# Kernel tuning notes

Hardware: AMD Instinct MI355X
Metric: run time of the kernel (lower is better)

Reference implementation:

```python
import jax, jax.numpy as jnp
import numpy as np

N_NODES = 100000
N_EDGES = 1600000
IN_DIM = 64
OUT_DIM = 64
K_HEADS = 4
HEAD_DIM = OUT_DIM // K_HEADS


def setup_inputs() -> dict:
    key = jax.random.key(0)
    ks = jax.random.split(key, 12)
    x = jax.random.normal(ks[0], (N_NODES, IN_DIM), dtype=jnp.float32)
    edge_index = jax.random.randint(ks[1], (2, N_EDGES), 0, N_NODES, dtype=jnp.int64)
    edge_sign = jax.random.randint(ks[2], (N_EDGES,), 0, 2, dtype=jnp.int64)
    s = 1.0 / np.sqrt(IN_DIM)
    Wl_w = jax.random.uniform(ks[3], (OUT_DIM, IN_DIM), minval=-s, maxval=s, dtype=jnp.float32)
    Wl_b = jax.random.uniform(ks[4], (OUT_DIM,), minval=-s, maxval=s, dtype=jnp.float32)
    sign_tab = jax.random.normal(ks[5], (2, HEAD_DIM), dtype=jnp.float32)
    so = 1.0 / np.sqrt(OUT_DIM)
    Wh_w = jax.random.uniform(ks[6], (OUT_DIM, OUT_DIM), minval=-so, maxval=so, dtype=jnp.float32)
    Wh_b = jax.random.uniform(ks[7], (OUT_DIM,), minval=-so, maxval=so, dtype=jnp.float32)
    mlp_w1 = jax.random.uniform(ks[8], (OUT_DIM, OUT_DIM), minval=-so, maxval=so, dtype=jnp.float32)
    mlp_b1 = jax.random.uniform(ks[9], (OUT_DIM,), minval=-so, maxval=so, dtype=jnp.float32)
    mlp_w2 = jax.random.uniform(ks[10], (OUT_DIM, OUT_DIM), minval=-so, maxval=so, dtype=jnp.float32)
    mlp_b2 = jax.random.uniform(ks[11], (OUT_DIM,), minval=-so, maxval=so, dtype=jnp.float32)
    eps = jnp.zeros((1,), dtype=jnp.float32)
    return {"x": x, "edge_index": edge_index, "edge_sign": edge_sign,
            "Wl_w": Wl_w, "Wl_b": Wl_b, "sign_tab": sign_tab,
            "Wh_w": Wh_w, "Wh_b": Wh_b, "mlp_w1": mlp_w1, "mlp_b1": mlp_b1,
            "mlp_w2": mlp_w2, "mlp_b2": mlp_b2, "eps": eps}


def reference(x, edge_index, edge_sign, Wl_w, Wl_b, sign_tab, Wh_w, Wh_b,
              mlp_w1, mlp_b1, mlp_w2, mlp_b2, eps):
    N = x.shape[0]
    row, col = edge_index[0], edge_index[1]
    h = x @ Wl_w.T + Wl_b                              # [N, out_dim]
    hr = h.reshape(N, K_HEADS, HEAD_DIM)               # [N, K, hd]
    h_i = hr[row]                                      # [E, K, hd]
    h_j = hr[col]                                      # [E, K, hd]
    s_emb = sign_tab[edge_sign][:, None, :]            # [E, 1, hd]
    score = jnp.sum(h_i * h_j * s_emb, axis=-1)        # [E, K]
    # segment softmax over edges grouped by target node (row)
    mx = jax.ops.segment_max(score, row, num_segments=N)
    mx = jnp.where(jnp.isfinite(mx), mx, 0.0)          # empty segments -> 0
    ex = jnp.exp(score - mx[row])                      # [E, K]
    den = jax.ops.segment_sum(ex, row, num_segments=N)
    alpha = ex / (den[row] + 1e-16)                    # [E, K]
    # scatter-add weighted messages per head (vectorized over heads)
    msg = h_j * alpha[:, :, None]                      # [E, K, hd]
    aggr = jax.ops.segment_sum(msg, row, num_segments=N)  # [N, K, hd]
    m_l = aggr.reshape(N, OUT_DIM) @ Wh_w.T + Wh_b
    z = (1.0 + eps) * h + m_l
    hid = jax.nn.relu(z @ mlp_w1.T + mlp_b1)
    return hid @ mlp_w2.T + mlp_b2
```

## Files before the change

### kernel.cpp

```cpp
#include <hip/hip_runtime.h>

#define DIM 64
#define NBUCK 256
#define BSHIFT 9
#define BCAP 12288
#define CHUNK 4096

typedef __attribute__((ext_vector_type(4))) float f32x4;
typedef __attribute__((ext_vector_type(2))) float f32x2v;
typedef __attribute__((ext_vector_type(8))) short short8;

#define MFMA16(a, b, c) __builtin_amdgcn_mfma_f32_16x16x32_bf16(a, b, c, 0, 0, 0)

template <int CTRL>
__device__ __forceinline__ float qperm(float v) {
    return __int_as_float(__builtin_amdgcn_update_dpp(
        0, __float_as_int(v), CTRL, 0xF, 0xF, true));
}

__device__ __forceinline__ void cvt8(const float* f, short8& hi, short8& lo) {
#pragma unroll
    for (int e = 0; e < 8; ++e) {
        const unsigned u = __float_as_uint(f[e]);
        hi[e] = (short)(u >> 16);
        const float hf = __uint_as_float(u & 0xFFFF0000u);
        lo[e] = (short)(__float_as_uint(f[e] - hf) >> 16);
    }
}

__device__ __forceinline__ unsigned short bf16rne(float f) {
    const unsigned u = __float_as_uint(f);
    return (unsigned short)((u + 0x7FFFu + ((u >> 16) & 1u)) >> 16);
}

__global__ __launch_bounds__(256) void prep_kernel(
    const float* __restrict__ Wl, const float* __restrict__ Wh,
    const float* __restrict__ W1, const float* __restrict__ W2,
    short8* __restrict__ wf, int* __restrict__ bcursor,
    int* __restrict__ edata, int* __restrict__ offsets, int N, int E)
{
    const int tid = threadIdx.x;
    bcursor[tid] = 0;
    edata[E + tid] = 0;
    edata[E + 256 + tid] = 0;
    if (tid == 0) offsets[N] = E;
    const int m = tid >> 6, l = tid & 63;
    const float* W = (m == 0) ? Wl : (m == 1) ? Wh : (m == 2) ? W1 : W2;
    const int o = l & 15;
    const int kg = (l >> 4) * 8;
#pragma unroll
    for (int t = 0; t < 4; ++t)
#pragma unroll
        for (int s = 0; s < 2; ++s) {
            float f[8];
#pragma unroll
            for (int e = 0; e < 8; ++e)
                f[e] = W[(o + 16 * t) * DIM + 32 * s + kg + e];
            short8 hi, lo;
            cvt8(f, hi, lo);
            const int base = (((m * 4 + t) * 2 + s) * 2);
            wf[(base + 0) * 64 + l] = hi;
            wf[(base + 1) * 64 + l] = lo;
        }
}

__global__ __launch_bounds__(256, 3) void gemmbin_kernel(
    const float* __restrict__ x, const short8* __restrict__ wf,
    const float* __restrict__ bias, float* __restrict__ h,
    unsigned short* __restrict__ hb, int N,
    const int* __restrict__ ei, const int* __restrict__ sgn,
    int* __restrict__ bcursor, int* __restrict__ records, int E, int NB)
{
    if (blockIdx.x & 1) {
        const int l = threadIdx.x & 63;
        const int gw = (blockIdx.x >> 1) * 4 + (threadIdx.x >> 6);
        const int nw = NB * 4;
        const int nstrips = (N + 15) >> 4;
        const int lr = l & 15, lk = (l >> 4) * 8, lrow4 = (l >> 4) * 4;

        short8 wh_[4][2], wl_[4][2];
#pragma unroll
        for (int t = 0; t < 4; ++t)
#pragma unroll
            for (int s = 0; s < 2; ++s) {
                wh_[t][s] = wf[(((0 * 4 + t) * 2 + s) * 2 + 0) * 64 + l];
                wl_[t][s] = wf[(((0 * 4 + t) * 2 + s) * 2 + 1) * 64 + l];
            }
        float b4[4];
#pragma unroll
        for (int t = 0; t < 4; ++t) b4[t] = bias[lr + 16 * t];

        for (int strip = gw; strip < nstrips; strip += nw) {
            const int rbase = strip * 16;
            const int arow = min(rbase + lr, N - 1);
            short8 ah[2], al[2];
#pragma unroll
            for (int s = 0; s < 2; ++s) {
                const float4 p0 = *reinterpret_cast<const float4*>(x + (size_t)arow * DIM + 32 * s + lk);
                const float4 p1 = *reinterpret_cast<const float4*>(x + (size_t)arow * DIM + 32 * s + lk + 4);
                float f[8] = {p0.x, p0.y, p0.z, p0.w, p1.x, p1.y, p1.z, p1.w};
                cvt8(f, ah[s], al[s]);
            }
            f32x4 acc[4];
#pragma unroll
            for (int t = 0; t < 4; ++t) acc[t] = (f32x4){b4[t], b4[t], b4[t], b4[t]};
#pragma unroll
            for (int s = 0; s < 2; ++s) {
#pragma unroll
                for (int t = 0; t < 4; ++t) acc[t] = MFMA16(ah[s], wh_[t][s], acc[t]);
#pragma unroll
                for (int t = 0; t < 4; ++t) acc[t] = MFMA16(ah[s], wl_[t][s], acc[t]);
#pragma unroll
                for (int t = 0; t < 4; ++t) acc[t] = MFMA16(al[s], wh_[t][s], acc[t]);
            }
#pragma unroll
            for (int t = 0; t < 4; ++t)
#pragma unroll
                for (int rg = 0; rg < 4; ++rg) {
                    const int row = rbase + lrow4 + rg;
                    if (row < N) {
                        h[(size_t)row * DIM + lr + 16 * t] = acc[t][rg];
                        hb[(size_t)row * DIM + lr + 16 * t] = bf16rne(acc[t][rg]);
                    }
                }
        }
    } else {
        const int tid = threadIdx.x;
        const int base = (blockIdx.x >> 1) * CHUNK;
        __shared__ int lcnt[NBUCK];
        __shared__ int lbase[NBUCK];
        lcnt[tid] = 0;
        __syncthreads();
        const int lim = min(CHUNK, E - base);
        if (lim == CHUNK && (E & 3) == 0) {
            int r[16];
#pragma unroll
            for (int j = 0; j < 4; ++j) {
                const int4 a = *(reinterpret_cast<const int4*>(ei + base) + tid * 4 + j);
                r[4*j+0]=a.x; r[4*j+1]=a.y; r[4*j+2]=a.z; r[4*j+3]=a.w;
            }
#pragma unroll
            for (int i = 0; i < 16; ++i) atomicAdd(&lcnt[r[i] >> BSHIFT], 1);
            __syncthreads();
            const int c = lcnt[tid];
            lbase[tid] = c ? atomicAdd(&bcursor[tid], c) : 0;
            lcnt[tid] = 0;
            __syncthreads();
            int cc[16], ss[16];
#pragma unroll
            for (int j = 0; j < 4; ++j) {
                const int4 a = *(reinterpret_cast<const int4*>(ei + E + base) + tid * 4 + j);
                cc[4*j+0]=a.x; cc[4*j+1]=a.y; cc[4*j+2]=a.z; cc[4*j+3]=a.w;
                const int4 s2 = *(reinterpret_cast<const int4*>(sgn + base) + tid * 4 + j);
                ss[4*j+0]=s2.x; ss[4*j+1]=s2.y; ss[4*j+2]=s2.z; ss[4*j+3]=s2.w;
            }
#pragma unroll
            for (int half = 0; half < 2; ++half) {
                int idx[8];
#pragma unroll
                for (int i = 0; i < 8; ++i) {
                    const int e8 = half * 8 + i;
                    const int bkt = r[e8] >> BSHIFT;
                    idx[i] = lbase[bkt] + atomicAdd(&lcnt[bkt], 1);
                }
#pragma unroll
                for (int i = 0; i < 8; ++i) {
                    const int e8 = half * 8 + i;
                    const int bkt = r[e8] >> BSHIFT;
                    records[bkt * BCAP + min(idx[i], BCAP - 1)] =
                        cc[e8] | (ss[e8] << 17) | ((r[e8] & 511) << 18);
                }
            }
        } else {
            for (int k = tid; k < lim; k += 256)
                atomicAdd(&lcnt[ei[base + k] >> BSHIFT], 1);
            __syncthreads();
            const int c = lcnt[tid];
            lbase[tid] = c ? atomicAdd(&bcursor[tid], c) : 0;
            lcnt[tid] = 0;
            __syncthreads();
            for (int k = tid; k < lim; k += 256) {
                const int e = base + k;
                const int rr = ei[e];
                const int cc2 = ei[E + e];
                const int s = sgn[e];
                const int b = rr >> BSHIFT;
                const int idx = min(lbase[b] + atomicAdd(&lcnt[b], 1), BCAP - 1);
                records[b * BCAP + idx] = cc2 | (s << 17) | ((rr & 511) << 18);
            }
        }
    }
}

__device__ __forceinline__ int wave_incl_scan(int v, int lane) {
#pragma unroll
    for (int off = 1; off < 64; off <<= 1) {
        int t = __shfl_up(v, (unsigned)off, 64);
        if (lane >= off) v += t;
    }
    return v;
}

__global__ __launch_bounds__(256) void build_kernel(
    const int* __restrict__ records, const int* __restrict__ bcursor,
    int* __restrict__ offsets, int* __restrict__ edata, int N)
{
    const int b = blockIdx.x;
    const int tid = threadIdx.x, lane = tid & 63, w = tid >> 6;
    const int nbase = b << BSHIFT;
    const int nn = min(512, N - nbase);
    if (nn <= 0) return;

    __shared__ int ncnt[512];
    __shared__ int wtot[8];
    __shared__ int csrb_l[NBUCK];
    __shared__ int stag[BCAP];

    {
        const int bv = min(bcursor[tid], BCAP);
        const int inc = wave_incl_scan(bv, lane);
        if (lane == 63) wtot[w] = inc;
        __syncthreads();
        int add = 0;
#pragma unroll
        for (int i = 0; i < 4; ++i)
            if (i < w) add += wtot[i];
        csrb_l[tid] = add + inc - bv;
        __syncthreads();
    }
    const int base_csr = csrb_l[b];
    const int cnt = min(bcursor[b], BCAP);
    const int* rec = records + b * BCAP;

    ncnt[tid] = 0; ncnt[256 + tid] = 0;
    __syncthreads();
    for (int i = tid; i < cnt; i += 256)
        atomicAdd(&ncnt[rec[i] >> 18], 1);
    __syncthreads();
    const int v0 = ncnt[tid], v1 = ncnt[256 + tid];
    const int i0 = wave_incl_scan(v0, lane);
    if (lane == 63) wtot[w] = i0;
    const int i1 = wave_incl_scan(v1, lane);
    if (lane == 63) wtot[4 + w] = i1;
    __syncthreads();
    int a0 = 0, a1 = 0;
#pragma unroll
    for (int i = 0; i < 4; ++i) {
        if (i < w) { a0 += wtot[i]; a1 += wtot[4 + i]; }
    }
    const int half = wtot[0] + wtot[1] + wtot[2] + wtot[3];
    const int e0 = a0 + i0 - v0;
    const int e1 = half + a1 + i1 - v1;
    if (tid < nn)       offsets[nbase + tid]       = base_csr + e0;
    if (256 + tid < nn) offsets[nbase + 256 + tid] = base_csr + e1;
    __syncthreads();
    ncnt[tid] = e0; ncnt[256 + tid] = e1;
    __syncthreads();
    for (int i = tid; i < cnt; i += 256) {
        const int rcd = rec[i];
        const int p = atomicAdd(&ncnt[rcd >> 18], 1);
        stag[p] = (rcd & 0x1FFFF) | (((rcd >> 17) & 1) << 20);
    }
    __syncthreads();
    for (int i = tid; i < cnt; i += 256)
        edata[base_csr + i] = stag[i];
}

__global__ __launch_bounds__(256) void attn_kernel(
    const float* __restrict__ h, const unsigned short* __restrict__ hb,
    const int* __restrict__ offsets, const int* __restrict__ edata,
    const float* __restrict__ sign_tab, float* __restrict__ aggr, int n)
{
    const int lane = threadIdx.x & 63;
    const int gl   = lane & 15;
    const int node = blockIdx.x * 16 + ((threadIdx.x >> 6) << 2) + (lane >> 4);
    const bool alive = node < n;
    const int nidx = alive ? node : 0;

    const int beg = offsets[nidx];
    const int deg = offsets[nidx + 1] - beg;

    const float4 hi = *reinterpret_cast<const float4*>(h + ((unsigned)nidx << 6) + (gl << 2));
    const float4 s0 = *reinterpret_cast<const float4*>(sign_tab + ((gl & 3) << 2));
    const float4 s1 = *reinterpret_cast<const float4*>(sign_tab + 16 + ((gl & 3) << 2));
    const f32x2v hs0a = {hi.x * s0.x, hi.y * s0.y};
    const f32x2v hs0b = {hi.z * s0.z, hi.w * s0.w};
    const f32x2v hs1a = {hi.x * s1.x, hi.y * s1.y};
    const f32x2v hs1b = {hi.z * s1.z, hi.w * s1.w};

    int maxdeg = max(deg, __shfl_xor(deg, 16, 64));
    maxdeg = max(maxdeg, __shfl_xor(maxdeg, 32, 64));

    float den = 0.f;
    f32x2v ma = {0.f, 0.f}, mb = {0.f, 0.f};
    const unsigned glb = (unsigned)(gl << 3);

    for (int e = 0; e < maxdeg; e += 8) {
        int pk[8];
#pragma unroll
        for (int u = 0; u < 8; ++u)
            pk[u] = edata[(unsigned)(beg + e + u)];
        uint2 v[8];
#pragma unroll
        for (int u = 0; u < 8; ++u) {
            unsigned off = (((unsigned)pk[u] & 0x1FFFFu) << 7) + glb;
            off = (e + u < deg) ? off : glb;
            v[u] = *reinterpret_cast<const uint2*>(
                reinterpret_cast<const char*>(hb) + off);
        }
#pragma unroll
        for (int u = 0; u < 8; ++u) {
            const f32x2v ha = {__uint_as_float(v[u].x << 16),
                               __uint_as_float(v[u].x & 0xFFFF0000u)};
            const f32x2v hc = {__uint_as_float(v[u].y << 16),
                               __uint_as_float(v[u].y & 0xFFFF0000u)};
            const bool sg = (pk[u] >> 20) & 1;
            const f32x2v wa = sg ? hs1a : hs0a;
            const f32x2v wb = sg ? hs1b : hs0b;
            const f32x2v p = wa * ha + wb * hc;
            float sc = p.x + p.y;
            sc += qperm<0xB1>(sc);
            sc += qperm<0x4E>(sc);
            const float ex = (e + u < deg) ? __expf(sc) : 0.f;
            den += ex;
            ma += ex * ha;
            mb += ex * hc;
        }
    }

    if (alive) {
        const float inv = 1.0f / (den + 1e-16f);
        float4 o = make_float4(ma.x * inv, ma.y * inv, mb.x * inv, mb.y * inv);
        *reinterpret_cast<float4*>(aggr + ((unsigned)node << 6) + (gl << 2)) = o;
    }
}

__global__ __launch_bounds__(256, 2) void tail_kernel(
    const float* __restrict__ aggr, const float* __restrict__ hres,
    const short8* __restrict__ wf,
    const float* __restrict__ bh, const float* __restrict__ b1,
    const float* __restrict__ b2, const float* __restrict__ eps,
    float* __restrict__ out, int N)
{
    __shared__ float zb[4][16 * 68];
    const int l = threadIdx.x & 63;
    const int w = threadIdx.x >> 6;
    const int gw = blockIdx.x * 4 + w;
    const int nw = gridDim.x * 4;
    const int nstrips = (N + 15) >> 4;
    const int lr = l & 15, lk = (l >> 4) * 8, lrow4 = (l >> 4) * 4;
    float* zw = zb[w];

    short8 whh[4][2], w1h[4][2], w2h[4][2];
#pragma unroll
    for (int t = 0; t < 4; ++t)
#pragma unroll
        for (int s = 0; s < 2; ++s) {
            whh[t][s] = wf[(((1 * 4 + t) * 2 + s) * 2 + 0) * 64 + l];
            w1h[t][s] = wf[(((2 * 4 + t) * 2 + s) * 2 + 0) * 64 + l];
            w2h[t][s] = wf[(((3 * 4 + t) * 2 + s) * 2 + 0) * 64 + l];
        }
    float bh4[4], b14[4], b24[4];
#pragma unroll
    for (int t = 0; t < 4; ++t) {
        bh4[t] = bh[lr + 16 * t];
        b14[t] = b1[lr + 16 * t];
        b24[t] = b2[lr + 16 * t];
    }
    const float escale = 1.0f + eps[0];

    for (int strip = gw; strip < nstrips; strip += nw) {
        const int rbase = strip * 16;

        float vh[4][4];
#pragma unroll
        for (int t = 0; t < 4; ++t)
#pragma unroll
            for (int rg = 0; rg < 4; ++rg)
                vh[t][rg] = hres[(size_t)min(rbase + lrow4 + rg, N - 1) * DIM + lr + 16 * t];

        const int arow = min(rbase + lr, N - 1);
        short8 ah[2], al[2];
#pragma unroll
        for (int s = 0; s < 2; ++s) {
            const float4 p0 = *reinterpret_cast<const float4*>(aggr + (size_t)arow * DIM + 32 * s + lk);
            const float4 p1 = *reinterpret_cast<const float4*>(aggr + (size_t)arow * DIM + 32 * s + lk + 4);
            float f[8] = {p0.x, p0.y, p0.z, p0.w, p1.x, p1.y, p1.z, p1.w};
            cvt8(f, ah[s], al[s]);
        }
        short8 lo_[4][2];
#pragma unroll
        for (int t = 0; t < 4; ++t)
#pragma unroll
            for (int s = 0; s < 2; ++s)
                lo_[t][s] = wf[(((1 * 4 + t) * 2 + s) * 2 + 1) * 64 + l];
        f32x4 acc[4];
#pragma unroll
        for (int t = 0; t < 4; ++t) acc[t] = (f32x4){bh4[t], bh4[t], bh4[t], bh4[t]};
#pragma unroll
        for (int s = 0; s < 2; ++s) {
#pragma unroll
            for (int t = 0; t < 4; ++t) acc[t] = MFMA16(ah[s], whh[t][s], acc[t]);
#pragma unroll
            for (int t = 0; t < 4; ++t) acc[t] = MFMA16(ah[s], lo_[t][s], acc[t]);
#pragma unroll
            for (int t = 0; t < 4; ++t) acc[t] = MFMA16(al[s], whh[t][s], acc[t]);
        }
#pragma unroll
        for (int t = 0; t < 4; ++t)
#pragma unroll
            for (int rg = 0; rg < 4; ++rg)
                zw[(lrow4 + rg) * 68 + lr + 16 * t] = fmaf(escale, vh[t][rg], acc[t][rg]);
        asm volatile("s_waitcnt lgkmcnt(0)" ::: "memory");

        short8 zh[2], zl[2];
#pragma unroll
        for (int s = 0; s < 2; ++s) {
            const float4 q0 = *reinterpret_cast<const float4*>(zw + lr * 68 + 32 * s + lk);
            const float4 q1 = *reinterpret_cast<const float4*>(zw + lr * 68 + 32 * s + lk + 4);
            float f[8] = {q0.x, q0.y, q0.z, q0.w, q1.x, q1.y, q1.z, q1.w};
            cvt8(f, zh[s], zl[s]);
        }
#pragma unroll
        for (int t = 0; t < 4; ++t)
#pragma unroll
            for (int s = 0; s < 2; ++s)
                lo_[t][s] = wf[(((2 * 4 + t) * 2 + s) * 2 + 1) * 64 + l];
#pragma unroll
        for (int t = 0; t < 4; ++t) acc[t] = (f32x4){b14[t], b14[t], b14[t], b14[t]};
#pragma unroll
        for (int s = 0; s < 2; ++s) {
#pragma unroll
            for (int t = 0; t < 4; ++t) acc[t] = MFMA16(zh[s], w1h[t][s], acc[t]);
#pragma unroll
            for (int t = 0; t < 4; ++t) acc[t] = MFMA16(zh[s], lo_[t][s], acc[t]);
#pragma unroll
            for (int t = 0; t < 4; ++t) acc[t] = MFMA16(zl[s], w1h[t][s], acc[t]);
        }
#pragma unroll
        for (int t = 0; t < 4; ++t)
#pragma unroll
            for (int rg = 0; rg < 4; ++rg)
                zw[(lrow4 + rg) * 68 + lr + 16 * t] = fmaxf(acc[t][rg], 0.f);
        asm volatile("s_waitcnt lgkmcnt(0)" ::: "memory");

        short8 hh[2], hl[2];
#pragma unroll
        for (int s = 0; s < 2; ++s) {
            const float4 q0 = *reinterpret_cast<const float4*>(zw + lr * 68 + 32 * s + lk);
            const float4 q1 = *reinterpret_cast<const float4*>(zw + lr * 68 + 32 * s + lk + 4);
            float f[8] = {q0.x, q0.y, q0.z, q0.w, q1.x, q1.y, q1.z, q1.w};
            cvt8(f, hh[s], hl[s]);
        }
#pragma unroll
        for (int t = 0; t < 4; ++t)
#pragma unroll
            for (int s = 0; s < 2; ++s)
                lo_[t][s] = wf[(((3 * 4 + t) * 2 + s) * 2 + 1) * 64 + l];
#pragma unroll
        for (int t = 0; t < 4; ++t) acc[t] = (f32x4){b24[t], b24[t], b24[t], b24[t]};
#pragma unroll
        for (int s = 0; s < 2; ++s) {
#pragma unroll
            for (int t = 0; t < 4; ++t) acc[t] = MFMA16(hh[s], w2h[t][s], acc[t]);
#pragma unroll
            for (int t = 0; t < 4; ++t) acc[t] = MFMA16(hh[s], lo_[t][s], acc[t]);
#pragma unroll
            for (int t = 0; t < 4; ++t) acc[t] = MFMA16(hl[s], w2h[t][s], acc[t]);
        }
#pragma unroll
        for (int t = 0; t < 4; ++t)
#pragma unroll
            for (int rg = 0; rg < 4; ++rg) {
                const int row = rbase + lrow4 + rg;
                if (row < N) out[(size_t)row * DIM + lr + 16 * t] = acc[t][rg];
            }
    }
}

extern "C" void kernel_launch(void* const* d_in, const int* in_sizes, int n_in,
                              void* d_out, int out_size, void* d_ws, size_t ws_size,
                              hipStream_t stream) {
    const float* x        = (const float*)d_in[0];
    const int*   ei       = (const int*)d_in[1];
    const int*   esign    = (const int*)d_in[2];
    const float* Wl_w     = (const float*)d_in[3];
    const float* Wl_b     = (const float*)d_in[4];
    const float* sign_tab = (const float*)d_in[5];
    const float* Wh_w     = (const float*)d_in[6];
    const float* Wh_b     = (const float*)d_in[7];
    const float* w1       = (const float*)d_in[8];
    const float* b1       = (const float*)d_in[9];
    const float* w2       = (const float*)d_in[10];
    const float* b2       = (const float*)d_in[11];
    const float* eps      = (const float*)d_in[12];
    float* out = (float*)d_out;

    const int N = in_sizes[0] / DIM;
    const int E = in_sizes[2];

    float* h       = (float*)d_ws;
    float* aggr    = h + (size_t)N * DIM;
    int*   records = (int*)aggr;
    int*   edata   = (int*)(aggr + (size_t)N * DIM);
    int*   bcursor = edata + (E + 520);
    int*   offsets = bcursor + NBUCK;
    short8* wf     = (short8*)(offsets + ((N + 1 + 3) & ~3));
    unsigned short* hb = (unsigned short*)d_out;

    const int NB = (E + CHUNK - 1) / CHUNK;

    prep_kernel<<<1, 256, 0, stream>>>(Wl_w, Wh_w, w1, w2, wf, bcursor,
                                       edata, offsets, N, E);

    gemmbin_kernel<<<2 * NB, 256, 0, stream>>>(x, wf, Wl_b, h, hb, N,
                                               ei, esign, bcursor, records, E, NB);

    build_kernel<<<NBUCK, 256, 0, stream>>>(records, bcursor, offsets, edata, N);

    attn_kernel<<<(N + 15) / 16, 256, 0, stream>>>(h, hb, offsets, edata, sign_tab, aggr, N);

    tail_kernel<<<512, 256, 0, stream>>>(aggr, h, wf, Wh_b, b1, b2, eps, out, N);
}
```

Baseline: 122.2 us.

## Fuse attention aggregation and MLP tail into one kernel via LDS staging

Merges the attention kernel and the tail GEMM kernel so each 16-node block keeps its aggregated rows in shared memory and runs the three 64x64 split-bf16 MFMA layers in place, with each wave owning one 16-column output tile. This removes the global write and re-read of the aggr buffer and one kernel launch. The bf16 copy of h moves from the output buffer into workspace to avoid aliasing with the fused output writes. In exchange, every block reloads weight fragments and uses extra block-wide barriers, and the tail work is no longer spread over a persistent grid.

Result: faster. 110.5 us (-9.6%).

```diff
diff --git a/kernel.cpp b/kernel.cpp
--- a/kernel.cpp
+++ b/kernel.cpp
@@ -266,15 +266,24 @@
         edata[base_csr + i] = stag[i];
 }
 
-__global__ __launch_bounds__(256) void attn_kernel(
+__global__ __launch_bounds__(256) void attntail_kernel(
     const float* __restrict__ h, const unsigned short* __restrict__ hb,
     const int* __restrict__ offsets, const int* __restrict__ edata,
-    const float* __restrict__ sign_tab, float* __restrict__ aggr, int n)
+    const float* __restrict__ sign_tab, const short8* __restrict__ wf,
+    const float* __restrict__ bh, const float* __restrict__ b1,
+    const float* __restrict__ b2, const float* __restrict__ eps,
+    float* __restrict__ out, int N)
 {
+    __shared__ float bufA[16 * 68];
+    __shared__ float bufB[16 * 68];
+
     const int lane = threadIdx.x & 63;
+    const int w    = threadIdx.x >> 6;
     const int gl   = lane & 15;
-    const int node = blockIdx.x * 16 + ((threadIdx.x >> 6) << 2) + (lane >> 4);
-    const bool alive = node < n;
+    const int g    = lane >> 4;
+    const int rbase = blockIdx.x * 16;
+    const int node  = rbase + (w << 2) + g;
+    const bool alive = node < N;
     const int nidx = alive ? node : 0;
 
     const int beg = offsets[nidx];
@@ -327,154 +336,92 @@
             mb += ex * hc;
         }
     }
-
-    if (alive) {
+    {
         const float inv = 1.0f / (den + 1e-16f);
-        float4 o = make_float4(ma.x * inv, ma.y * inv, mb.x * inv, mb.y * inv);
-        *reinterpret_cast<float4*>(aggr + ((unsigned)node << 6) + (gl << 2)) = o;
-    }
-}
-
-__global__ __launch_bounds__(256, 2) void tail_kernel(
-    const float* __restrict__ aggr, const float* __restrict__ hres,
-    const short8* __restrict__ wf,
-    const float* __restrict__ bh, const float* __restrict__ b1,
-    const float* __restrict__ b2, const float* __restrict__ eps,
-    float* __restrict__ out, int N)
-{
-    __shared__ float zb[4][16 * 68];
-    const int l = threadIdx.x & 63;
-    const int w = threadIdx.x >> 6;
-    const int gw = blockIdx.x * 4 + w;
-    const int nw = gridDim.x * 4;
-    const int nstrips = (N + 15) >> 4;
-    const int lr = l & 15, lk = (l >> 4) * 8, lrow4 = (l >> 4) * 4;
-    float* zw = zb[w];
-
-    short8 whh[4][2], w1h[4][2], w2h[4][2];
-#pragma unroll
-    for (int t = 0; t < 4; ++t)
-#pragma unroll
-        for (int s = 0; s < 2; ++s) {
-            whh[t][s] = wf[(((1 * 4 + t) * 2 + s) * 2 + 0) * 64 + l];
-            w1h[t][s] = wf[(((2 * 4 + t) * 2 + s) * 2 + 0) * 64 + l];
-            w2h[t][s] = wf[(((3 * 4 + t) * 2 + s) * 2 + 0) * 64 + l];
-        }
-    float bh4[4], b14[4], b24[4];
-#pragma unroll
-    for (int t = 0; t < 4; ++t) {
-        bh4[t] = bh[lr + 16 * t];
-        b14[t] = b1[lr + 16 * t];
-        b24[t] = b2[lr + 16 * t];
-    }
+        float* rowp = bufA + ((w << 2) + g) * 68 + (gl << 2);
+        rowp[0] = ma.x * inv; rowp[1] = ma.y * inv;
+        rowp[2] = mb.x * inv; rowp[3] = mb.y * inv;
+    }
+    __syncthreads();
+
+    const int lr = lane & 15, lk = (lane >> 4) * 8, lrow4 = (lane >> 4) * 4;
+    short8 f1h[2], f1l[2], f2h[2], f2l[2], f3h[2], f3l[2];
+#pragma unroll
+    for (int s = 0; s < 2; ++s) {
+        f1h[s] = wf[(((1 * 4 + w) * 2 + s) * 2 + 0) * 64 + lane];
+        f1l[s] = wf[(((1 * 4 + w) * 2 + s) * 2 + 1) * 64 + lane];
+        f2h[s] = wf[(((2 * 4 + w) * 2 + s) * 2 + 0) * 64 + lane];
+        f2l[s] = wf[(((2 * 4 + w) * 2 + s) * 2 + 1) * 64 + lane];
+        f3h[s] = wf[(((3 * 4 + w) * 2 + s) * 2 + 0) * 64 + lane];
+        f3l[s] = wf[(((3 * 4 + w) * 2 + s) * 2 + 1) * 64 + lane];
+    }
+    const float bhv = bh[lr + 16 * w];
+    const float b1v = b1[lr + 16 * w];
+    const float b2v = b2[lr + 16 * w];
     const float escale = 1.0f + eps[0];
 
-    for (int strip = gw; strip < nstrips; strip += nw) {
-        const int rbase = strip * 16;
-
-        float vh[4][4];
-#pragma unroll
-        for (int t = 0; t < 4; ++t)
-#pragma unroll
-            for (int rg = 0; rg < 4; ++rg)
-                vh[t][rg] = hres[(size_t)min(rbase + lrow4 + rg, N - 1) * DIM + lr + 16 * t];
-
-        const int arow = min(rbase + lr, N - 1);
-        short8 ah[2], al[2];
-#pragma unroll
-        for (int s = 0; s < 2; ++s) {
-            const float4 p0 = *reinterpret_cast<const float4*>(aggr + (size_t)arow * DIM + 32 * s + lk);
-            const float4 p1 = *reinterpret_cast<const float4*>(aggr + (size_t)arow * DIM + 32 * s + lk + 4);
-            float f[8] = {p0.x, p0.y, p0.z, p0.w, p1.x, p1.y, p1.z, p1.w};
-            cvt8(f, ah[s], al[s]);
-        }
-        short8 lo_[4][2];
-#pragma unroll
-        for (int t = 0; t < 4; ++t)
-#pragma unroll
-            for (int s = 0; s < 2; ++s)
-                lo_[t][s] = wf[(((1 * 4 + t) * 2 + s) * 2 + 1) * 64 + l];
-        f32x4 acc[4];
-#pragma unroll
-        for (int t = 0; t < 4; ++t) acc[t] = (f32x4){bh4[t], bh4[t], bh4[t], bh4[t]};
-#pragma unroll
-        for (int s = 0; s < 2; ++s) {
-#pragma unroll
-            for (int t = 0; t < 4; ++t) acc[t] = MFMA16(ah[s], whh[t][s], acc[t]);
-#pragma unroll
-            for (int t = 0; t < 4; ++t) acc[t] = MFMA16(ah[s], lo_[t][s], acc[t]);
-#pragma unroll
-            for (int t = 0; t < 4; ++t) acc[t] = MFMA16(al[s], whh[t][s], acc[t]);
-        }
-#pragma unroll
-        for (int t = 0; t < 4; ++t)
-#pragma unroll
-            for (int rg = 0; rg < 4; ++rg)
-                zw[(lrow4 + rg) * 68 + lr + 16 * t] = fmaf(escale, vh[t][rg], acc[t][rg]);
-        asm volatile("s_waitcnt lgkmcnt(0)" ::: "memory");
-
-        short8 zh[2], zl[2];
-#pragma unroll
-        for (int s = 0; s < 2; ++s) {
-            const float4 q0 = *reinterpret_cast<const float4*>(zw + lr * 68 + 32 * s + lk);
-            const float4 q1 = *reinterpret_cast<const float4*>(zw + lr * 68 + 32 * s + lk + 4);
-            float f[8] = {q0.x, q0.y, q0.z, q0.w, q1.x, q1.y, q1.z, q1.w};
-            cvt8(f, zh[s], zl[s]);
-        }
-#pragma unroll
-        for (int t = 0; t < 4; ++t)
-#pragma unroll
-            for (int s = 0; s < 2; ++s)
-                lo_[t][s] = wf[(((2 * 4 + t) * 2 + s) * 2 + 1) * 64 + l];
-#pragma unroll
-        for (int t = 0; t < 4; ++t) acc[t] = (f32x4){b14[t], b14[t], b14[t], b14[t]};
-#pragma unroll
-        for (int s = 0; s < 2; ++s) {
-#pragma unroll
-            for (int t = 0; t < 4; ++t) acc[t] = MFMA16(zh[s], w1h[t][s], acc[t]);
-#pragma unroll
-            for (int t = 0; t < 4; ++t) acc[t] = MFMA16(zh[s], lo_[t][s], acc[t]);
-#pragma unroll
-            for (int t = 0; t < 4; ++t) acc[t] = MFMA16(zl[s], w1h[t][s], acc[t]);
-        }
-#pragma unroll
-        for (int t = 0; t < 4; ++t)
-#pragma unroll
-            for (int rg = 0; rg < 4; ++rg)
-                zw[(lrow4 + rg) * 68 + lr + 16 * t] = fmaxf(acc[t][rg], 0.f);
-        asm volatile("s_waitcnt lgkmcnt(0)" ::: "memory");
-
-        short8 hh[2], hl[2];
-#pragma unroll
-        for (int s = 0; s < 2; ++s) {
-            const float4 q0 = *reinterpret_cast<const float4*>(zw + lr * 68 + 32 * s + lk);
-            const float4 q1 = *reinterpret_cast<const float4*>(zw + lr * 68 + 32 * s + lk + 4);
-            float f[8] = {q0.x, q0.y, q0.z, q0.w, q1.x, q1.y, q1.z, q1.w};
-            cvt8(f, hh[s], hl[s]);
-        }
-#pragma unroll
-        for (int t = 0; t < 4; ++t)
-#pragma unroll
-            for (int s = 0; s < 2; ++s)
-                lo_[t][s] = wf[(((3 * 4 + t) * 2 + s) * 2 + 1) * 64 + l];
-#pragma unroll
-        for (int t = 0; t < 4; ++t) acc[t] = (f32x4){b24[t], b24[t], b24[t], b24[t]};
-#pragma unroll
-        for (int s = 0; s < 2; ++s) {
-#pragma unroll
-            for (int t = 0; t < 4; ++t) acc[t] = MFMA16(hh[s], w2h[t][s], acc[t]);
-#pragma unroll
-            for (int t = 0; t < 4; ++t) acc[t] = MFMA16(hh[s], lo_[t][s], acc[t]);
-#pragma unroll
-            for (int t = 0; t < 4; ++t) acc[t] = MFMA16(hl[s], w2h[t][s], acc[t]);
-        }
-#pragma unroll
-        for (int t = 0; t < 4; ++t)
-#pragma unroll
-            for (int rg = 0; rg < 4; ++rg) {
-                const int row = rbase + lrow4 + rg;
-                if (row < N) out[(size_t)row * DIM + lr + 16 * t] = acc[t][rg];
-            }
+    float vh[4];
+#pragma unroll
+    for (int rg = 0; rg < 4; ++rg)
+        vh[rg] = h[(size_t)min(rbase + lrow4 + rg, N - 1) * DIM + lr + 16 * w];
+
+    short8 ah[2], al[2];
+#pragma unroll
+    for (int s = 0; s < 2; ++s) {
+        float f[8];
+#pragma unroll
+        for (int e = 0; e < 8; ++e) f[e] = bufA[lr * 68 + 32 * s + lk + e];
+        cvt8(f, ah[s], al[s]);
+    }
+    f32x4 acc = (f32x4){bhv, bhv, bhv, bhv};
+#pragma unroll
+    for (int s = 0; s < 2; ++s) {
+        acc = MFMA16(ah[s], f1h[s], acc);
+        acc = MFMA16(ah[s], f1l[s], acc);
+        acc = MFMA16(al[s], f1h[s], acc);
+    }
+#pragma unroll
+    for (int rg = 0; rg < 4; ++rg)
+        bufB[(lrow4 + rg) * 68 + lr + 16 * w] = fmaf(escale, vh[rg], acc[rg]);
+    __syncthreads();
+
+#pragma unroll
+    for (int s = 0; s < 2; ++s) {
+        float f[8];
+#pragma unroll
+        for (int e = 0; e < 8; ++e) f[e] = bufB[lr * 68 + 32 * s + lk + e];
+        cvt8(f, ah[s], al[s]);
+    }
+    acc = (f32x4){b1v, b1v, b1v, b1v};
+#pragma unroll
+    for (int s = 0; s < 2; ++s) {
+        acc = MFMA16(ah[s], f2h[s], acc);
+        acc = MFMA16(ah[s], f2l[s], acc);
+        acc = MFMA16(al[s], f2h[s], acc);
+    }
+#pragma unroll
+    for (int rg = 0; rg < 4; ++rg)
+        bufA[(lrow4 + rg) * 68 + lr + 16 * w] = fmaxf(acc[rg], 0.f);
+    __syncthreads();
+
+#pragma unroll
+    for (int s = 0; s < 2; ++s) {
+        float f[8];
+#pragma unroll
+        for (int e = 0; e < 8; ++e) f[e] = bufA[lr * 68 + 32 * s + lk + e];
+        cvt8(f, ah[s], al[s]);
+    }
+    acc = (f32x4){b2v, b2v, b2v, b2v};
+#pragma unroll
+    for (int s = 0; s < 2; ++s) {
+        acc = MFMA16(ah[s], f3h[s], acc);
+        acc = MFMA16(ah[s], f3l[s], acc);
+        acc = MFMA16(al[s], f3h[s], acc);
+    }
+#pragma unroll
+    for (int rg = 0; rg < 4; ++rg) {
+        const int row = rbase + lrow4 + rg;
+        if (row < N) out[(size_t)row * DIM + lr + 16 * w] = acc[rg];
     }
 }
 
@@ -498,17 +445,15 @@
 
     const int N = in_sizes[0] / DIM;
     const int E = in_sizes[2];
-
-    float* h       = (float*)d_ws;
-    float* aggr    = h + (size_t)N * DIM;
-    int*   records = (int*)aggr;
-    int*   edata   = (int*)(aggr + (size_t)N * DIM);
-    int*   bcursor = edata + (E + 520);
-    int*   offsets = bcursor + NBUCK;
-    short8* wf     = (short8*)(offsets + ((N + 1 + 3) & ~3));
-    unsigned short* hb = (unsigned short*)d_out;
-
     const int NB = (E + CHUNK - 1) / CHUNK;
+
+    float* h            = (float*)d_ws;
+    unsigned short* hb  = (unsigned short*)(h + (size_t)N * DIM);
+    int*   records      = (int*)(hb + (size_t)N * DIM);
+    int*   edata        = records + NBUCK * BCAP;
+    int*   bcursor      = edata + (E + 520);
+    int*   offsets      = bcursor + NBUCK;
+    short8* wf          = (short8*)(offsets + ((N + 1 + 3) & ~3));
 
     prep_kernel<<<1, 256, 0, stream>>>(Wl_w, Wh_w, w1, w2, wf, bcursor,
                                        edata, offsets, N, E);
@@ -518,7 +463,6 @@
 
     build_kernel<<<NBUCK, 256, 0, stream>>>(records, bcursor, offsets, edata, N);
 
-    attn_kernel<<<(N + 15) / 16, 256, 0, stream>>>(h, hb, offsets, edata, sign_tab, aggr, N);
-
-    tail_kernel<<<512, 256, 0, stream>>>(aggr, h, wf, Wh_b, b1, b2, eps, out, N);
-}
+    attntail_kernel<<<(N + 15) / 16, 256, 0, stream>>>(
+        h, hb, offsets, edata, sign_tab, wf, Wh_b, b1, b2, eps, out, N);
+}
```
